# Performance work log

Hardware: AMD Instinct MI355X
Metric: run time of the kernel (lower is better)

The kernel has to match this reference:

```python
import jax, jax.numpy as jnp
import numpy as np

# Fixed architecture constants from AlgelogicNetwork.__init__
M, J, I, L, W = 4, 2, 3, 2, 9
B = 1048576  # batch size (only free dim)


def setup_inputs() -> dict:
    key = jax.random.key(0)
    ks = jax.random.split(key, 7)
    state = jax.random.normal(ks[0], (B, W * L), dtype=jnp.float32)
    # rule.constants ~ U(-1, 1), rule.gammas ~ U(0, 1), stacked over M rules
    constants = jax.random.uniform(ks[1], (M, J, L), minval=-1.0, maxval=1.0, dtype=jnp.float32)
    gammas = jax.random.uniform(ks[2], (M, J, L), dtype=jnp.float32)
    # body Linears (L -> I), one per (rule m, premise j); head Linear (I -> L) per rule
    W_body = jax.random.normal(ks[3], (M, J, I, L), dtype=jnp.float32) * 0.5
    b_body = jax.random.normal(ks[4], (M, J, I), dtype=jnp.float32) * 0.1
    W_head = jax.random.normal(ks[5], (M, L, I), dtype=jnp.float32) * 0.5
    b_head = jax.random.normal(ks[6], (M, L), dtype=jnp.float32) * 0.1
    return {
        "state": state,
        "constants": constants,
        "gammas": gammas,
        "W_body": W_body,
        "b_body": b_body,
        "W_head": W_head,
        "b_head": b_head,
    }


def reference(state, constants, gammas, W_body, b_body, W_head, b_head):
    s = state.reshape(-1, W, L)                       # [B, W, L]
    g = jnp.clip(gammas, 0.0, 1.0)                    # sigmoid() in source = clamp; [M, J, L]
    wgt = 1.0 - g                                     # [M, J, L]

    # match_scores[m,j,b,w] = sum_l (1-g[m,j,l]) * (const[m,j,l] - s[b,w,l])^2
    # L=2 fixed: unroll over l to avoid a [M,J,B,W,L] intermediate
    ms = sum(
        wgt[:, :, l, None, None]
        * (constants[:, :, l, None, None] - s[None, None, :, :, l]) ** 2
        for l in range(L)
    )                                                  # [M, J, B, W]

    attn = jax.nn.softmax(-ms, axis=-1)                # softmax over W positions (temperature=1)
    best = jnp.einsum('mjbw,bwl->mjbl', attn, s)       # soft-gathered propositions
    match_quality = jnp.sum(attn * ms, axis=-1).sum(axis=1)   # [M, B], summed over premises j

    captured = jnp.einsum('mjbl,mjil->mjbi', best, W_body) + b_body[:, :, None, :]  # body Linear
    g_avg = g.mean(axis=-1)                            # [M, J]
    captured_vars = jnp.einsum('mj,mjbi->mbi', g_avg, captured)                     # [M, B, I]

    rule_out = jnp.einsum('mbi,mli->mbl', captured_vars, W_head) + b_head[:, None, :]  # [M, B, L]

    # similarity[m,b,w] = -sum_l (rule_out[m,b,l] - s[b,w,l])^2
    sim = -jnp.sum((rule_out[:, :, None, :] - s[None]) ** 2, axis=-1)  # [M, B, W]
    confidence = jnp.exp(-match_quality)               # [M, B]
    return jnp.einsum('mb,mbw->bw', confidence, sim)   # [B, W]
```

## Files before the change

### kernel.cpp

```cpp
#include <hip/hip_runtime.h>

namespace {
constexpr int kM = 4, kJ = 2, kI = 3, kL = 2, kW = 9;
constexpr float kInvLn2 = 1.4426950408889634f;

typedef float v2f __attribute__((ext_vector_type(2)));

__device__ __forceinline__ float fexp2(float x) { return __builtin_amdgcn_exp2f(x); }

__global__ __launch_bounds__(256) void algelogic_fused(
    const float* __restrict__ state,
    const float* __restrict__ constants,
    const float* __restrict__ gammas,
    const float* __restrict__ W_body,
    const float* __restrict__ b_body,
    const float* __restrict__ W_head,
    const float* __restrict__ b_head,
    float* __restrict__ out) {
  __shared__ float sdp[80];
  const int t = threadIdx.x;

  if (t < 8) {
    const int mj = t, m = t >> 1, j = t & 1;
    const float g0 = fminf(fmaxf(gammas[mj * kL + 0], 0.f), 1.f);
    const float g1 = fminf(fmaxf(gammas[mj * kL + 1], 0.f), 1.f);
    const float w0 = 1.f - g0, w1 = 1.f - g1;
    const float c0 = constants[mj * kL + 0], c1 = constants[mj * kL + 1];
    const float gavg = 0.5f * (g0 + g1);
    float* base = sdp + m * 18;
    base[0 * 2 + j] = (w0 * c0 * c0 + w1 * c1 * c1) * kInvLn2;
    base[1 * 2 + j] = -2.f * w0 * c0 * kInvLn2;
    base[2 * 2 + j] = -2.f * w1 * c1 * kInvLn2;
    base[3 * 2 + j] = w0 * kInvLn2;
    base[4 * 2 + j] = w1 * kInvLn2;
    for (int l = 0; l < kL; ++l)
      for (int lp = 0; lp < kL; ++lp) {
        float acc = 0.f;
        for (int i = 0; i < kI; ++i)
          acc += W_head[(m * kL + l) * kI + i] * W_body[(mj * kI + i) * kL + lp];
        base[(5 + l * kL + lp) * 2 + j] = gavg * acc;
      }
  } else if (t < 12) {
    const int m = t - 8;
    for (int l = 0; l < kL; ++l) {
      float d = b_head[m * kL + l];
      for (int j = 0; j < kJ; ++j) {
        const int mj = m * kJ + j;
        const float g0 = fminf(fmaxf(gammas[mj * kL + 0], 0.f), 1.f);
        const float g1 = fminf(fmaxf(gammas[mj * kL + 1], 0.f), 1.f);
        const float gavg = 0.5f * (g0 + g1);
        float acc = 0.f;
        for (int i = 0; i < kI; ++i)
          acc += W_head[(m * kL + l) * kI + i] * b_body[mj * kI + i];
        d += gavg * acc;
      }
      sdp[72 + m * kL + l] = d;
    }
  }
  __syncthreads();

  const int b = blockIdx.x * 256 + t;
  const float* srow = state + (size_t)b * (kW * kL);

  v2f sv[kW], qv[kW];
#pragma unroll
  for (int w = 0; w < kW; ++w) {
    const float2 v = *reinterpret_cast<const float2*>(srow + 2 * w);
    v2f s; s.x = v.x; s.y = v.y;
    sv[w] = s;
    qv[w] = s * s;
  }

  float Cs = 0.f, X0 = 0.f, X1 = 0.f, K = 0.f;
#pragma unroll
  for (int m = 0; m < kM; ++m) {
    const v2f* pp = reinterpret_cast<const v2f*>(sdp + m * 18);
    const v2f A = pp[0], B0 = pp[1], B1 = pp[2], w0 = pp[3], w1 = pp[4];

    v2f msP[kW];
    v2f mn = {3.4e38f, 3.4e38f};
#pragma unroll
    for (int w = 0; w < kW; ++w) {
      const float s0w = sv[w].x, s1w = sv[w].y;
      const float q0w = qv[w].x, q1w = qv[w].y;
      v2f v = A + B0 * s0w;
      v += w0 * q0w;
      v += B1 * s1w;
      v += w1 * q1w;
      msP[w] = v;
      mn = __builtin_elementwise_min(mn, v);
    }

    v2f psum = {0.f, 0.f}, pb0 = {0.f, 0.f}, pb1 = {0.f, 0.f}, pmq = {0.f, 0.f};
#pragma unroll
    for (int w = 0; w < kW; ++w) {
      const v2f d = mn - msP[w];
      v2f e; e.x = fexp2(d.x); e.y = fexp2(d.y);
      psum += e;
      pb0 += e * sv[w].x;
      pb1 += e * sv[w].y;
      pmq += e * msP[w];
    }

    v2f rinv;
    rinv.x = __builtin_amdgcn_rcpf(psum.x);
    rinv.y = __builtin_amdgcn_rcpf(psum.y);
    const v2f bb0 = pb0 * rinv, bb1 = pb1 * rinv;
    const v2f mqP = pmq * rinv;
    const float mq2 = mqP.x + mqP.y;
    const float conf = fexp2(-mq2);

    const v2f C00 = pp[5], C01 = pp[6], C10 = pp[7], C11 = pp[8];
    const v2f t0 = C00 * bb0 + C01 * bb1;
    const v2f t1 = C10 * bb0 + C11 * bb1;
    const float r0 = sdp[72 + m * 2 + 0] + t0.x + t0.y;
    const float r1 = sdp[72 + m * 2 + 1] + t1.x + t1.y;

    Cs += conf;
    X0 = fmaf(conf, r0, X0);
    X1 = fmaf(conf, r1, X1);
    K = fmaf(conf, fmaf(r0, r0, r1 * r1), K);
  }

  const float X02 = 2.f * X0, X12 = 2.f * X1;
  float* orow = out + (size_t)b * kW;
#pragma unroll
  for (int w = 0; w < kW; ++w) {
    const float qs = qv[w].x + qv[w].y;
    orow[w] = fmaf(X02, sv[w].x, fmaf(X12, sv[w].y, fmaf(-Cs, qs, -K)));
  }
}
}

extern "C" void kernel_launch(void* const* d_in, const int* in_sizes, int n_in,
                              void* d_out, int out_size, void* d_ws, size_t ws_size,
                              hipStream_t stream) {
  const float* state     = (const float*)d_in[0];
  const float* constants = (const float*)d_in[1];
  const float* gammas    = (const float*)d_in[2];
  const float* W_body    = (const float*)d_in[3];
  const float* b_body    = (const float*)d_in[4];
  const float* W_head    = (const float*)d_in[5];
  const float* b_head    = (const float*)d_in[6];
  float* out = (float*)d_out;

  const int B = in_sizes[0] / (kW * kL);
  hipLaunchKernelGGL(algelogic_fused, dim3(B / 256), dim3(256), 0, stream,
                     state, constants, gammas, W_body, b_body, W_head, b_head, out);
}
```

Measured before the change: 35.56 us.

## Split parameter prep into separate kernel and shrink main kernel blocks

Moves the per-block parameter folding into a one-block prep kernel that writes 80 floats to workspace; the main kernel just copies them into shared memory, overlapping that copy with the state loads before the barrier. Block size drops to 128 with launch bounds asking for 6 blocks per CU, and the squared-state registers are dropped in favour of recomputing them via a Horner-style form. This removes redundant prep work in every block and reduces register pressure, at the cost of an extra kernel launch and a dependent workspace read.

```diff
diff --git a/kernel.cpp b/kernel.cpp
--- a/kernel.cpp
+++ b/kernel.cpp
@@ -8,18 +8,14 @@
 
 __device__ __forceinline__ float fexp2(float x) { return __builtin_amdgcn_exp2f(x); }
 
-__global__ __launch_bounds__(256) void algelogic_fused(
-    const float* __restrict__ state,
-    const float* __restrict__ constants,
-    const float* __restrict__ gammas,
-    const float* __restrict__ W_body,
-    const float* __restrict__ b_body,
-    const float* __restrict__ W_head,
-    const float* __restrict__ b_head,
-    float* __restrict__ out) {
-  __shared__ float sdp[80];
+__global__ void prep_kernel(const float* __restrict__ constants,
+                            const float* __restrict__ gammas,
+                            const float* __restrict__ W_body,
+                            const float* __restrict__ b_body,
+                            const float* __restrict__ W_head,
+                            const float* __restrict__ b_head,
+                            float* __restrict__ dp) {
   const int t = threadIdx.x;
-
   if (t < 8) {
     const int mj = t, m = t >> 1, j = t & 1;
     const float g0 = fminf(fmaxf(gammas[mj * kL + 0], 0.f), 1.f);
@@ -27,7 +23,7 @@
     const float w0 = 1.f - g0, w1 = 1.f - g1;
     const float c0 = constants[mj * kL + 0], c1 = constants[mj * kL + 1];
     const float gavg = 0.5f * (g0 + g1);
-    float* base = sdp + m * 18;
+    float* base = dp + m * 18;
     base[0 * 2 + j] = (w0 * c0 * c0 + w1 * c1 * c1) * kInvLn2;
     base[1 * 2 + j] = -2.f * w0 * c0 * kInvLn2;
     base[2 * 2 + j] = -2.f * w1 * c1 * kInvLn2;
@@ -54,22 +50,29 @@
           acc += W_head[(m * kL + l) * kI + i] * b_body[mj * kI + i];
         d += gavg * acc;
       }
-      sdp[72 + m * kL + l] = d;
+      dp[72 + m * kL + l] = d;
     }
   }
-  __syncthreads();
+}
 
-  const int b = blockIdx.x * 256 + t;
+__global__ __launch_bounds__(128, 6) void algelogic_main(
+    const float* __restrict__ state, const float* __restrict__ dp,
+    float* __restrict__ out) {
+  __shared__ float sdp[80];
+  const int t = threadIdx.x;
+
+  if (t < 80) sdp[t] = dp[t];
+
+  const int b = blockIdx.x * 128 + t;
   const float* srow = state + (size_t)b * (kW * kL);
-
-  v2f sv[kW], qv[kW];
+  v2f sv[kW];
 #pragma unroll
   for (int w = 0; w < kW; ++w) {
     const float2 v = *reinterpret_cast<const float2*>(srow + 2 * w);
     v2f s; s.x = v.x; s.y = v.y;
     sv[w] = s;
-    qv[w] = s * s;
   }
+  __syncthreads();
 
   float Cs = 0.f, X0 = 0.f, X1 = 0.f, K = 0.f;
 #pragma unroll
@@ -82,11 +85,10 @@
 #pragma unroll
     for (int w = 0; w < kW; ++w) {
       const float s0w = sv[w].x, s1w = sv[w].y;
-      const float q0w = qv[w].x, q1w = qv[w].y;
-      v2f v = A + B0 * s0w;
-      v += w0 * q0w;
-      v += B1 * s1w;
-      v += w1 * q1w;
+      const v2f t0 = B0 + w0 * s0w;
+      const v2f t1 = B1 + w1 * s1w;
+      v2f v = A + t0 * s0w;
+      v += t1 * s1w;
       msP[w] = v;
       mn = __builtin_elementwise_min(mn, v);
     }
@@ -126,7 +128,8 @@
   float* orow = out + (size_t)b * kW;
 #pragma unroll
   for (int w = 0; w < kW; ++w) {
-    const float qs = qv[w].x + qv[w].y;
+    const v2f q = sv[w] * sv[w];
+    const float qs = q.x + q.y;
     orow[w] = fmaf(X02, sv[w].x, fmaf(X12, sv[w].y, fmaf(-Cs, qs, -K)));
   }
 }
@@ -143,8 +146,11 @@
   const float* W_head    = (const float*)d_in[5];
   const float* b_head    = (const float*)d_in[6];
   float* out = (float*)d_out;
+  float* dp  = (float*)d_ws;
 
   const int B = in_sizes[0] / (kW * kL);
-  hipLaunchKernelGGL(algelogic_fused, dim3(B / 256), dim3(256), 0, stream,
-                     state, constants, gammas, W_body, b_body, W_head, b_head, out);
+  hipLaunchKernelGGL(prep_kernel, dim3(1), dim3(64), 0, stream,
+                     constants, gammas, W_body, b_body, W_head, b_head, dp);
+  hipLaunchKernelGGL(algelogic_main, dim3(B / 128), dim3(128), 0, stream,
+                     state, dp, out);
 }
```

Result: no change. 35.99 us (+1.2%).
